# Kernel tuning notes

Hardware: AMD Instinct MI355X
Metric: run time of the kernel (lower is better)

Reference implementation:

```python
import jax, jax.numpy as jnp
import numpy as np

B = 4096          # batch
L = 4096          # lattice_size (64x64)
N = L // 2        # n_masked
H = 2048          # hidden_size


def setup_inputs() -> dict:
    key = jax.random.key(0)
    ks = jax.random.split(key, 4)
    scale = 0.02  # small init so exp(s) stays tame (s is already bounded by 2*tanh)
    x = jax.random.normal(ks[0], (B, L), dtype=jnp.float32)
    W1 = jax.random.normal(ks[1], (N, H), dtype=jnp.float32) * scale
    b1 = jnp.zeros((H,), jnp.float32)
    W2 = jax.random.normal(ks[2], (H, H), dtype=jnp.float32) * scale
    b2 = jnp.zeros((H,), jnp.float32)
    W3 = jax.random.normal(ks[3], (H, 2 * N), dtype=jnp.float32) * scale
    b3 = jnp.zeros((2 * N,), jnp.float32)
    # checkerboard mask: even sites frozen (masked), odd sites transformed
    idx_masked = jnp.arange(0, L, 2, dtype=jnp.int32)
    idx_unmasked = jnp.arange(1, L, 2, dtype=jnp.int32)
    return {"x": x, "W1": W1, "b1": b1, "W2": W2, "b2": b2,
            "W3": W3, "b3": b3,
            "idx_masked": idx_masked, "idx_unmasked": idx_unmasked}


def reference(x, W1, b1, W2, b2, W3, b3, idx_masked, idx_unmasked):
    # gather frozen half: (B, N)
    x_m = x[:, idx_masked]
    # 3-layer MLP with LeakyReLU(0.2)
    h = jax.nn.leaky_relu(x_m @ W1 + b1, negative_slope=0.2)
    h = jax.nn.leaky_relu(h @ W2 + b2, negative_slope=0.2)
    out = h @ W3 + b3                      # (B, 2N)
    s, t = out[:, :N], out[:, N:]
    s = 2.0 * jnp.tanh(s)
    # affine transform of the unmasked half, scatter back
    x_u = x[:, idx_unmasked]
    y_u = x_u * jnp.exp(s) + t
    y = x.at[:, idx_unmasked].set(y_u)
    log_det = s.sum(axis=1)                # (B,)
    return y, log_det
```

## Files before the change

kernel.cpp:

```cpp
#include <hip/hip_runtime.h>
#include <hip/hip_bf16.h>
#include <stdint.h>

#define MROWS 4096
#define LFULL 4096
#define NHALF 2048
#define HDIM  2048

typedef __bf16 bf16x8 __attribute__((ext_vector_type(8)));
typedef float  f32x4  __attribute__((ext_vector_type(4)));
typedef unsigned short u16x8 __attribute__((ext_vector_type(8)));

__device__ __forceinline__ unsigned short f2bf(float f) {
    __hip_bfloat16 h = __float2bfloat16(f);
    return __builtin_bit_cast(unsigned short, h);
}
__device__ __forceinline__ float bf2f(unsigned short u) {
    return __builtin_bit_cast(float, (uint32_t)u << 16);
}
__device__ __forceinline__ float fast_tanh(float x) {
    float ax = fabsf(x);
    float e  = __expf(-2.0f * ax);
    float t  = (1.0f - e) / (1.0f + e);
    return copysignf(t, x);
}

__device__ __forceinline__ void gload_lds16(const void* g, void* l) {
    __builtin_amdgcn_global_load_lds(
        (const __attribute__((address_space(1))) uint32_t*)g,
        (__attribute__((address_space(3))) uint32_t*)l,
        16, 0, 0);
}

#define WAIT_LGKM0 do { asm volatile("s_waitcnt lgkmcnt(0)" ::: "memory"); __builtin_amdgcn_sched_barrier(0); } while (0)
#define BARRIER    do { __builtin_amdgcn_s_barrier(); __builtin_amdgcn_sched_barrier(0); } while (0)

__device__ __forceinline__ void stage64(const __hip_bfloat16* g, int ldK, char* ldsHalf, int tid) {
    int r = tid >> 3, c = tid & 7;
    int sc = c ^ (r & 7);
    gload_lds16(g + (size_t)r * ldK + sc * 8, ldsHalf + r * 128 + c * 16);
}

__device__ __forceinline__ bf16x8 ldsRead(const char* tileBase, int row, int colByte) {
    int off = row * 128 + (colByte ^ ((row & 7) << 4));
    return *(const bf16x8*)(tileBase + off);
}

__global__ __launch_bounds__(256)
void cast_x_kernel(const float* __restrict__ x, __hip_bfloat16* __restrict__ xm)
{
    size_t t = (size_t)blockIdx.x * 256 + threadIdx.x;
    size_t r = t >> 8;
    int    c = (int)(t & 255);
    const float4* xp = (const float4*)(x + r * LFULL + (size_t)c * 16);
    float4 a = xp[0], b = xp[1], d = xp[2], e = xp[3];
    u16x8 v;
    v[0] = f2bf(a.x); v[1] = f2bf(a.z);
    v[2] = f2bf(b.x); v[3] = f2bf(b.z);
    v[4] = f2bf(d.x); v[5] = f2bf(d.z);
    v[6] = f2bf(e.x); v[7] = f2bf(e.z);
    *(u16x8*)(xm + r * NHALF + (size_t)c * 8) = v;
}

__global__ __launch_bounds__(256)
void transpose_cast_kernel(const float* __restrict__ W, __hip_bfloat16* __restrict__ WT,
                           int K, int N)
{
    __shared__ unsigned short lds[64][66];
    const int t  = threadIdx.x;
    const int k0 = blockIdx.y * 64;
    const int n0 = blockIdx.x * 64;

    #pragma unroll
    for (int it = 0; it < 4; ++it) {
        int kl = it * 16 + (t >> 4);
        int nl = (t & 15) * 4;
        float4 v = *(const float4*)(W + (size_t)(k0 + kl) * N + n0 + nl);
        lds[kl][nl + 0] = f2bf(v.x);
        lds[kl][nl + 1] = f2bf(v.y);
        lds[kl][nl + 2] = f2bf(v.z);
        lds[kl][nl + 3] = f2bf(v.w);
    }
    __syncthreads();

    int nl = t >> 2;
    int kc = (t & 3) * 16;
    unsigned short tmp[16];
    #pragma unroll
    for (int j = 0; j < 16; ++j) tmp[j] = lds[kc + j][nl];
    u16x8* dst = (u16x8*)(WT + (size_t)(n0 + nl) * K + k0 + kc);
    dst[0] = *(u16x8*)&tmp[0];
    dst[1] = *(u16x8*)&tmp[8];
}

template<int BM, int BN, bool RELU>
__global__ __launch_bounds__(512, 2)
void gemm8p(const __hip_bfloat16* __restrict__ A,
            const __hip_bfloat16* __restrict__ BT,
            const float* __restrict__ bias,
            __hip_bfloat16* __restrict__ C,
            int M, int K, int Nout)
{
    constexpr int MF = BM / 32;
    constexpr int NF = BN / 64;
    constexpr int MH = MF / 2;
    constexpr int NH = NF / 2;
    constexpr int LA = BM / 128;
    constexpr int LB = BN / 128;
    constexpr int BUFB = (BM + BN) * 128;
    __shared__ __align__(1024) char lds[2 * BUFB];

    const int tid  = threadIdx.x;
    const int wave = tid >> 6, lane = tid & 63;
    const int wm = wave >> 2, wn = wave & 3;
    const int l15 = lane & 15, lhi = lane >> 4;

    const int nwg = gridDim.x;
    const int bid = blockIdx.x;
    const int wg  = (bid & 7) * (nwg >> 3) + (bid >> 3);
    const int NBN = Nout / BN;
    const int bm = wg / NBN, bn = wg % NBN;

    const int NT = K >> 6;
    const __hip_bfloat16* gA = A  + (size_t)(bm * BM) * K;
    const __hip_bfloat16* gB = BT + (size_t)(bn * BN) * K;

    {
        char* A0b = lds;
        char* B0b = lds + BM * 128;
        char* B1b = lds + BUFB + BM * 128;
        #pragma unroll
        for (int s = 0; s < LB; ++s) stage64(gB + (size_t)(s * 64) * K, K, B0b + s * 64 * 128, tid);
        #pragma unroll
        for (int s = 0; s < LB; ++s) stage64(gB + (size_t)(BN / 2 + s * 64) * K, K, B0b + (BN / 2 + s * 64) * 128, tid);
        #pragma unroll
        for (int s = 0; s < LA; ++s) stage64(gA + (size_t)(s * 64) * K, K, A0b + s * 64 * 128, tid);
        #pragma unroll
        for (int s = 0; s < LA; ++s) stage64(gA + (size_t)(BM / 2 + s * 64) * K, K, A0b + (BM / 2 + s * 64) * 128, tid);
        #pragma unroll
        for (int s = 0; s < LB; ++s) stage64(gB + (size_t)(s * 64) * K + 64, K, B1b + s * 64 * 128, tid);
        #pragma unroll
        for (int s = 0; s < LB; ++s) stage64(gB + (size_t)(BN / 2 + s * 64) * K + 64, K, B1b + (BN / 2 + s * 64) * 128, tid);
    }
    asm volatile("s_waitcnt vmcnt(4)" ::: "memory");
    __builtin_amdgcn_sched_barrier(0);
    BARRIER;

    bf16x8 af[MH][2], bf0[NH][2], bf1[NH][2];
    f32x4 acc[MF][NF] = {};

    const int arow0 = wm * (BM / 2) + l15;
    const int brow0 = wn * (BN / 4) + l15;
    const int cb = lhi * 16;

    for (int t = 0; t < NT; ++t) {
        char* Ab  = lds + (t & 1) * BUFB;
        char* Bb  = Ab + BM * 128;
        char* AbO = lds + ((t & 1) ^ 1) * BUFB;

        #pragma unroll
        for (int m = 0; m < MH; ++m)
            #pragma unroll
            for (int kk = 0; kk < 2; ++kk)
                af[m][kk] = ldsRead(Ab, arow0 + m * 16, kk * 64 + cb);
        #pragma unroll
        for (int n = 0; n < NH; ++n)
            #pragma unroll
            for (int kk = 0; kk < 2; ++kk)
                bf0[n][kk] = ldsRead(Bb, brow0 + n * 16, kk * 64 + cb);
        if (t + 1 < NT) {
            #pragma unroll
            for (int s = 0; s < LA; ++s)
                stage64(gA + (size_t)(s * 64) * K + (size_t)(t + 1) * 64, K, AbO + s * 64 * 128, tid);
        }
        BARRIER;
        WAIT_LGKM0;
        __builtin_amdgcn_s_setprio(1);
        #pragma unroll
        for (int m = 0; m < MH; ++m)
            #pragma unroll
            for (int n = 0; n < NH; ++n)
                #pragma unroll
                for (int kk = 0; kk < 2; ++kk)
                    acc[m][n] = __builtin_amdgcn_mfma_f32_16x16x32_bf16(af[m][kk], bf0[n][kk], acc[m][n], 0, 0, 0);
        __builtin_amdgcn_s_setprio(0);
        BARRIER;

        #pragma unroll
        for (int n = 0; n < NH; ++n)
            #pragma unroll
            for (int kk = 0; kk < 2; ++kk)
                bf1[n][kk] = ldsRead(Bb, brow0 + (NH + n) * 16, kk * 64 + cb);
        if (t + 1 < NT) {
            #pragma unroll
            for (int s = 0; s < LA; ++s)
                stage64(gA + (size_t)(BM / 2 + s * 64) * K + (size_t)(t + 1) * 64, K, AbO + (BM / 2 + s * 64) * 128, tid);
        }
        BARRIER;
        WAIT_LGKM0;
        __builtin_amdgcn_s_setprio(1);
        #pragma unroll
        for (int m = 0; m < MH; ++m)
            #pragma unroll
            for (int n = 0; n < NH; ++n)
                #pragma unroll
                for (int kk = 0; kk < 2; ++kk)
                    acc[m][NH + n] = __builtin_amdgcn_mfma_f32_16x16x32_bf16(af[m][kk], bf1[n][kk], acc[m][NH + n], 0, 0, 0);
        __builtin_amdgcn_s_setprio(0);
        BARRIER;

        #pragma unroll
        for (int m = 0; m < MH; ++m)
            #pragma unroll
            for (int kk = 0; kk < 2; ++kk)
                af[m][kk] = ldsRead(Ab, arow0 + (MH + m) * 16, kk * 64 + cb);
        if (t + 2 < NT) {
            #pragma unroll
            for (int s = 0; s < LB; ++s)
                stage64(gB + (size_t)(s * 64) * K + (size_t)(t + 2) * 64, K, Bb + s * 64 * 128, tid);
        }
        BARRIER;
        WAIT_LGKM0;
        __builtin_amdgcn_s_setprio(1);
        #pragma unroll
        for (int m = 0; m < MH; ++m)
            #pragma unroll
            for (int n = 0; n < NH; ++n)
                #pragma unroll
                for (int kk = 0; kk < 2; ++kk)
                    acc[MH + m][n] = __builtin_amdgcn_mfma_f32_16x16x32_bf16(af[m][kk], bf0[n][kk], acc[MH + m][n], 0, 0, 0);
        __builtin_amdgcn_s_setprio(0);
        BARRIER;

        if (t + 2 < NT) {
            #pragma unroll
            for (int s = 0; s < LB; ++s)
                stage64(gB + (size_t)(BN / 2 + s * 64) * K + (size_t)(t + 2) * 64, K, Bb + (BN / 2 + s * 64) * 128, tid);
        }
        BARRIER;
        __builtin_amdgcn_s_setprio(1);
        #pragma unroll
        for (int m = 0; m < MH; ++m)
            #pragma unroll
            for (int n = 0; n < NH; ++n)
                #pragma unroll
                for (int kk = 0; kk < 2; ++kk)
                    acc[MH + m][NH + n] = __builtin_amdgcn_mfma_f32_16x16x32_bf16(af[m][kk], bf1[n][kk], acc[MH + m][NH + n], 0, 0, 0);
        __builtin_amdgcn_s_setprio(0);
        if (t + 2 < NT) {
            asm volatile("s_waitcnt vmcnt(4)" ::: "memory");
        } else if (t + 1 < NT) {
            asm volatile("s_waitcnt vmcnt(0)" ::: "memory");
        }
        __builtin_amdgcn_sched_barrier(0);
        BARRIER;
    }

    const int crow0 = bm * BM + wm * (BM / 2) + lhi * 4;
    const int ccol0 = bn * BN + wn * (BN / 4) + l15;
    #pragma unroll
    for (int m = 0; m < MF; ++m) {
        #pragma unroll
        for (int n = 0; n < NF; ++n) {
            int col = ccol0 + n * 16;
            float bv = bias[col];
            #pragma unroll
            for (int r = 0; r < 4; ++r) {
                int row = crow0 + m * 16 + r;
                float v = acc[m][n][r] + bv;
                if (RELU) v = (v > 0.0f) ? v : 0.2f * v;
                C[(size_t)row * Nout + col] = __float2bfloat16(v);
            }
        }
    }
}

__global__ __launch_bounds__(256)
void epilogue_kernel(const float* __restrict__ x,
                     const __hip_bfloat16* __restrict__ outb,
                     float* __restrict__ y, float* __restrict__ ld)
{
    const int i = blockIdx.x;
    const int t = threadIdx.x;
    const __hip_bfloat16* orow = outb + (size_t)i * LFULL;
    const float* xrow = x + (size_t)i * LFULL;
    float* yrow = y + (size_t)i * LFULL;

    const int j0 = t * 8;
    u16x8 sv = *(const u16x8*)(orow + j0);
    u16x8 tv = *(const u16x8*)(orow + NHALF + j0);

    float part = 0.0f;
    #pragma unroll
    for (int u = 0; u < 8; u += 2) {
        float4 xv = *(const float4*)(xrow + 2 * (j0 + u));
        float s0 = bf2f(sv[u]),     s1 = bf2f(sv[u + 1]);
        float t0 = bf2f(tv[u]),     t1 = bf2f(tv[u + 1]);
        float a0 = 2.0f * fast_tanh(s0);
        float a1 = 2.0f * fast_tanh(s1);
        part += a0 + a1;
        float4 yv;
        yv.x = xv.x;  yv.y = xv.y * __expf(a0) + t0;
        yv.z = xv.z;  yv.w = xv.w * __expf(a1) + t1;
        *(float4*)(yrow + 2 * (j0 + u)) = yv;
    }

    #pragma unroll
    for (int off = 32; off; off >>= 1) part += __shfl_down(part, off, 64);
    __shared__ float red[4];
    if ((t & 63) == 0) red[t >> 6] = part;
    __syncthreads();
    if (t == 0) ld[i] = red[0] + red[1] + red[2] + red[3];
}

extern "C" void kernel_launch(void* const* d_in, const int* in_sizes, int n_in,
                              void* d_out, int out_size, void* d_ws, size_t ws_size,
                              hipStream_t stream)
{
    const float* x  = (const float*)d_in[0];
    const float* W1 = (const float*)d_in[1];
    const float* b1 = (const float*)d_in[2];
    const float* W2 = (const float*)d_in[3];
    const float* b2 = (const float*)d_in[4];
    const float* W3 = (const float*)d_in[5];
    const float* b3 = (const float*)d_in[6];

    char* ws = (char*)d_ws;
    const size_t MB = 1u << 20;
    __hip_bfloat16* W3T  = (__hip_bfloat16*)(ws);
    __hip_bfloat16* h2   = (__hip_bfloat16*)(ws + 16 * MB);
    __hip_bfloat16* xmb  = (__hip_bfloat16*)(ws + 32 * MB);
    __hip_bfloat16* W1T  = (__hip_bfloat16*)(ws + 48 * MB);
    __hip_bfloat16* W2T  = (__hip_bfloat16*)(ws + 56 * MB);
    __hip_bfloat16* h1   = (__hip_bfloat16*)(ws + 64 * MB);
    __hip_bfloat16* outb = (__hip_bfloat16*)(ws + 32 * MB);

    float* y  = (float*)d_out;
    float* ld = y + (size_t)MROWS * LFULL;

    cast_x_kernel<<<4096, 256, 0, stream>>>(x, xmb);
    transpose_cast_kernel<<<dim3(32, 32), 256, 0, stream>>>(W1, W1T, HDIM, HDIM);
    transpose_cast_kernel<<<dim3(32, 32), 256, 0, stream>>>(W2, W2T, HDIM, HDIM);
    transpose_cast_kernel<<<dim3(64, 32), 256, 0, stream>>>(W3, W3T, HDIM, LFULL);

    gemm8p<128, 256, true ><<<dim3(256), dim3(512), 0, stream>>>(xmb, W1T, b1, h1, MROWS, HDIM, HDIM);
    gemm8p<128, 256, true ><<<dim3(256), dim3(512), 0, stream>>>(h1,  W2T, b2, h2, MROWS, HDIM, HDIM);
    gemm8p<256, 256, false><<<dim3(256), dim3(512), 0, stream>>>(h2,  W3T, b3, outb, MROWS, HDIM, LFULL);

    epilogue_kernel<<<4096, 256, 0, stream>>>(x, outb, y, ld);
}
```

Before: 218.9 us.

## Software-pipeline LDS fragment reads one phase ahead of MFMA blocks in GEMM loop

Restructures the GEMM main loop so the A and B register fragments for the next quadrant, and for the next K-tile, are read from LDS before the preceding MFMA block runs, rather than just before their own use. The explicit lgkmcnt(0) waits are removed so the compiler's own waits let LDS reads overlap matrix math. This reorders barriers and prefetch points, adding register pressure and tighter correctness conditions on buffer reuse in exchange for hiding LDS latency.

```diff
diff --git a/kernel.cpp b/kernel.cpp
--- a/kernel.cpp
+++ b/kernel.cpp
@@ -32,8 +32,8 @@
         16, 0, 0);
 }
 
-#define WAIT_LGKM0 do { asm volatile("s_waitcnt lgkmcnt(0)" ::: "memory"); __builtin_amdgcn_sched_barrier(0); } while (0)
-#define BARRIER    do { __builtin_amdgcn_s_barrier(); __builtin_amdgcn_sched_barrier(0); } while (0)
+#define SBAR    __builtin_amdgcn_sched_barrier(0)
+#define BARRIER do { __builtin_amdgcn_s_barrier(); SBAR; } while (0)
 
 __device__ __forceinline__ void stage64(const __hip_bfloat16* g, int ldK, char* ldsHalf, int tid) {
     int r = tid >> 3, c = tid & 7;
@@ -143,7 +143,7 @@
         for (int s = 0; s < LB; ++s) stage64(gB + (size_t)(BN / 2 + s * 64) * K + 64, K, B1b + (BN / 2 + s * 64) * 128, tid);
     }
     asm volatile("s_waitcnt vmcnt(4)" ::: "memory");
-    __builtin_amdgcn_sched_barrier(0);
+    SBAR;
     BARRIER;
 
     bf16x8 af[MH][2], bf0[NH][2], bf1[NH][2];
@@ -152,39 +152,24 @@
     const int arow0 = wm * (BM / 2) + l15;
     const int brow0 = wn * (BN / 4) + l15;
     const int cb = lhi * 16;
+
+    #pragma unroll
+    for (int m = 0; m < MH; ++m)
+        #pragma unroll
+        for (int kk = 0; kk < 2; ++kk)
+            af[m][kk] = ldsRead(lds, arow0 + m * 16, kk * 64 + cb);
+    #pragma unroll
+    for (int n = 0; n < NH; ++n)
+        #pragma unroll
+        for (int kk = 0; kk < 2; ++kk)
+            bf0[n][kk] = ldsRead(lds + BM * 128, brow0 + n * 16, kk * 64 + cb);
+    SBAR;
 
     for (int t = 0; t < NT; ++t) {
         char* Ab  = lds + (t & 1) * BUFB;
         char* Bb  = Ab + BM * 128;
         char* AbO = lds + ((t & 1) ^ 1) * BUFB;
-
-        #pragma unroll
-        for (int m = 0; m < MH; ++m)
-            #pragma unroll
-            for (int kk = 0; kk < 2; ++kk)
-                af[m][kk] = ldsRead(Ab, arow0 + m * 16, kk * 64 + cb);
-        #pragma unroll
-        for (int n = 0; n < NH; ++n)
-            #pragma unroll
-            for (int kk = 0; kk < 2; ++kk)
-                bf0[n][kk] = ldsRead(Bb, brow0 + n * 16, kk * 64 + cb);
-        if (t + 1 < NT) {
-            #pragma unroll
-            for (int s = 0; s < LA; ++s)
-                stage64(gA + (size_t)(s * 64) * K + (size_t)(t + 1) * 64, K, AbO + s * 64 * 128, tid);
-        }
-        BARRIER;
-        WAIT_LGKM0;
-        __builtin_amdgcn_s_setprio(1);
-        #pragma unroll
-        for (int m = 0; m < MH; ++m)
-            #pragma unroll
-            for (int n = 0; n < NH; ++n)
-                #pragma unroll
-                for (int kk = 0; kk < 2; ++kk)
-                    acc[m][n] = __builtin_amdgcn_mfma_f32_16x16x32_bf16(af[m][kk], bf0[n][kk], acc[m][n], 0, 0, 0);
-        __builtin_amdgcn_s_setprio(0);
-        BARRIER;
+        char* BbO = AbO + BM * 128;
 
         #pragma unroll
         for (int n = 0; n < NH; ++n)
@@ -194,10 +179,26 @@
         if (t + 1 < NT) {
             #pragma unroll
             for (int s = 0; s < LA; ++s)
+                stage64(gA + (size_t)(s * 64) * K + (size_t)(t + 1) * 64, K, AbO + s * 64 * 128, tid);
+        }
+        BARRIER;
+        __builtin_amdgcn_s_setprio(1);
+        #pragma unroll
+        for (int m = 0; m < MH; ++m)
+            #pragma unroll
+            for (int n = 0; n < NH; ++n)
+                #pragma unroll
+                for (int kk = 0; kk < 2; ++kk)
+                    acc[m][n] = __builtin_amdgcn_mfma_f32_16x16x32_bf16(af[m][kk], bf0[n][kk], acc[m][n], 0, 0, 0);
+        __builtin_amdgcn_s_setprio(0);
+        BARRIER;
+
+        if (t + 1 < NT) {
+            #pragma unroll
+            for (int s = 0; s < LA; ++s)
                 stage64(gA + (size_t)(BM / 2 + s * 64) * K + (size_t)(t + 1) * 64, K, AbO + (BM / 2 + s * 64) * 128, tid);
         }
         BARRIER;
-        WAIT_LGKM0;
         __builtin_amdgcn_s_setprio(1);
         #pragma unroll
         for (int m = 0; m < MH; ++m)
@@ -207,20 +208,20 @@
                 for (int kk = 0; kk < 2; ++kk)
                     acc[m][NH + n] = __builtin_amdgcn_mfma_f32_16x16x32_bf16(af[m][kk], bf1[n][kk], acc[m][NH + n], 0, 0, 0);
         __builtin_amdgcn_s_setprio(0);
-        BARRIER;
-
+        SBAR;
         #pragma unroll
         for (int m = 0; m < MH; ++m)
             #pragma unroll
             for (int kk = 0; kk < 2; ++kk)
                 af[m][kk] = ldsRead(Ab, arow0 + (MH + m) * 16, kk * 64 + cb);
+        BARRIER;
+
         if (t + 2 < NT) {
             #pragma unroll
             for (int s = 0; s < LB; ++s)
                 stage64(gB + (size_t)(s * 64) * K + (size_t)(t + 2) * 64, K, Bb + s * 64 * 128, tid);
         }
         BARRIER;
-        WAIT_LGKM0;
         __builtin_amdgcn_s_setprio(1);
         #pragma unroll
         for (int m = 0; m < MH; ++m)
@@ -237,22 +238,37 @@
             for (int s = 0; s < LB; ++s)
                 stage64(gB + (size_t)(BN / 2 + s * 64) * K + (size_t)(t + 2) * 64, K, Bb + (BN / 2 + s * 64) * 128, tid);
         }
-        BARRIER;
-        __builtin_amdgcn_s_setprio(1);
-        #pragma unroll
-        for (int m = 0; m < MH; ++m)
-            #pragma unroll
-            for (int n = 0; n < NH; ++n)
-                #pragma unroll
-                for (int kk = 0; kk < 2; ++kk)
-                    acc[MH + m][NH + n] = __builtin_amdgcn_mfma_f32_16x16x32_bf16(af[m][kk], bf1[n][kk], acc[MH + m][NH + n], 0, 0, 0);
-        __builtin_amdgcn_s_setprio(0);
         if (t + 2 < NT) {
             asm volatile("s_waitcnt vmcnt(4)" ::: "memory");
         } else if (t + 1 < NT) {
             asm volatile("s_waitcnt vmcnt(0)" ::: "memory");
         }
-        __builtin_amdgcn_sched_barrier(0);
+        SBAR;
+        if (t + 1 < NT) {
+            #pragma unroll
+            for (int n = 0; n < NH; ++n)
+                #pragma unroll
+                for (int kk = 0; kk < 2; ++kk)
+                    bf0[n][kk] = ldsRead(BbO, brow0 + n * 16, kk * 64 + cb);
+        }
+        BARRIER;
+        __builtin_amdgcn_s_setprio(1);
+        #pragma unroll
+        for (int m = 0; m < MH; ++m)
+            #pragma unroll
+            for (int n = 0; n < NH; ++n)
+                #pragma unroll
+                for (int kk = 0; kk < 2; ++kk)
+                    acc[MH + m][NH + n] = __builtin_amdgcn_mfma_f32_16x16x32_bf16(af[m][kk], bf1[n][kk], acc[MH + m][NH + n], 0, 0, 0);
+        __builtin_amdgcn_s_setprio(0);
+        SBAR;
+        if (t + 1 < NT) {
+            #pragma unroll
+            for (int m = 0; m < MH; ++m)
+                #pragma unroll
+                for (int kk = 0; kk < 2; ++kk)
+                    af[m][kk] = ldsRead(AbO, arow0 + m * 16, kk * 64 + cb);
+        }
         BARRIER;
     }
 
```

Measured after the change: 218.7 us. About the same (-0.1%).
